# Kernel optimization log

Measured on AMD Instinct MI355X. Metric: run time of the kernel, lower is better.

Reference implementation:

```python
import jax, jax.numpy as jnp
import numpy as np

N = 50000      # nodes
E = 800000     # edges (avg degree 16)
F_IN = 256     # input feature dim
H, D = 4, 32   # heads, per-head dim
HD = H * D
K = 25000      # SAGPool keeps ceil(0.5*N) nodes
C = 2          # classes
SLOPE = 0.4
NEG = -1e9

def _gat(x, src, dst, valid, n, W, b, al, ar):
    # DGL GATConv: fc -> per-head attn logits -> edge softmax over dst -> weighted sum
    h = (x @ W).reshape(-1, H, D)                      # [n,H,D]
    el = jnp.einsum('nhd,hd->nh', h, al)
    er = jnp.einsum('nhd,hd->nh', h, ar)
    e = jax.nn.leaky_relu(el[src] + er[dst], SLOPE)    # [E,H]
    e = jnp.where(valid[:, None], e, NEG)
    m = jnp.maximum(jax.ops.segment_max(e, dst, num_segments=n), NEG)
    ex = jnp.exp(e - m[dst]) * valid[:, None].astype(x.dtype)
    s = jax.ops.segment_sum(ex, dst, num_segments=n)
    alpha = ex / jnp.maximum(s[dst], 1e-16)            # [E,H] edge softmax
    out = jax.ops.segment_sum(alpha[:, :, None] * h[src], dst, num_segments=n)
    return out + b.reshape(1, H, D), alpha

def _sagpool(x, src, dst, valid, n, k, Wc, bc):
    # score = GraphConv(in,1) with symmetric norm; keep top-k nodes, scale by tanh(score)
    vf = valid.astype(x.dtype)
    deg_o = jnp.maximum(jax.ops.segment_sum(vf, src, num_segments=n), 1.0)
    deg_i = jnp.maximum(jax.ops.segment_sum(vf, dst, num_segments=n), 1.0)
    h = (x @ Wc) * (deg_o ** -0.5)[:, None]
    agg = jax.ops.segment_sum(h[src] * vf[:, None], dst, num_segments=n)
    score = (agg * (deg_i ** -0.5)[:, None] + bc)[:, 0]   # [n]
    vals, perm = jax.lax.top_k(score, k)
    xk = x[perm] * jnp.tanh(vals)[:, None]                # [k,F]
    new_id = jnp.full((n,), -1, jnp.int32).at[perm].set(jnp.arange(k, dtype=jnp.int32))
    ns, nd = new_id[src], new_id[dst]
    nv = valid & (ns >= 0) & (nd >= 0)                    # edges fully inside subgraph
    return xk, jnp.where(nv, ns, 0), jnp.where(nv, nd, 0), nv

def setup_inputs():
    key = jax.random.key(0)
    k = jax.random.split(key, 18)
    rn = lambda i, shape, scale: jax.random.normal(k[i], shape, jnp.float32) * scale
    return {
        "feature": rn(0, (N, F_IN), 1.0),
        "strength": jax.random.uniform(k[1], (E,), dtype=jnp.float32),
        "W0": rn(2, (F_IN, HD), F_IN ** -0.5), "b0": jnp.zeros((HD,), jnp.float32),
        "al0": rn(3, (H, D), 0.1), "ar0": rn(4, (H, D), 0.1),
        "Wc0": rn(5, (HD, 1), HD ** -0.5), "bc0": jnp.zeros((1,), jnp.float32),
        "W1": rn(6, (HD, HD), HD ** -0.5), "b1": jnp.zeros((HD,), jnp.float32),
        "al1": rn(7, (H, D), 0.1), "ar1": rn(8, (H, D), 0.1),
        "gate_W": rn(9, (D, 1), D ** -0.5), "gate_b": jnp.zeros((1,), jnp.float32),
        "cls_W": rn(10, (D, C), D ** -0.5), "cls_b": jnp.zeros((C,), jnp.float32),
        "src": jax.random.randint(k[11], (E,), 0, N, dtype=jnp.int32),
        "dst": jax.random.randint(k[12], (E,), 0, N, dtype=jnp.int32),
    }

def reference(feature, strength, W0, b0, al0, ar0, Wc0, bc0, W1, b1, al1, ar1,
              gate_W, gate_b, cls_W, cls_b, src, dst):
    valid0 = jnp.ones((E,), bool)
    h0, _ = _gat(feature, src, dst, valid0, N, W0, b0, al0, ar0)
    x = h0.reshape(N, HD)                                  # flatten(1)
    x1, s1, d1, v1 = _sagpool(x, src, dst, valid0, N, K, Wc0, bc0)
    h1, atten = _gat(x1, s1, d1, v1, K, W1, b1, al1, ar1)  # get_attention=True
    strength1 = strength * v1.astype(strength.dtype)       # edata carried into subgraph (masked)
    res = h1.mean(axis=1)                                  # [K,D] mean over heads
    gate = jax.nn.softmax(res @ gate_W + gate_b, axis=0)   # [K,1] GlobalAttentionPooling
    readout = jnp.sum(gate * res, axis=0, keepdims=True)   # [1,D]
    lbl_pred = readout @ cls_W + cls_b                     # [1,C]
    return (readout, lbl_pred, atten, strength1)
```

## Files before the change

### kernel.cpp

```cpp
#include <hip/hip_runtime.h>
#include <stdint.h>

#define NN 50000
#define EE 800000
#define FIN 256
#define HD 128
#define DD 32
#define KK 25000
#define SLOPEF 0.4f
#define NEGF (-1e9f)
#define ATT_OFF 34
#define STR_OFF (34 + EE * 4)
#define CW 128

__device__ __forceinline__ unsigned fkey(float x) {
    unsigned u = __float_as_uint(x);
    return (u & 0x80000000u) ? ~u : (u | 0x80000000u);
}
__device__ __forceinline__ float unfkey(unsigned k) {
    unsigned u = (k & 0x80000000u) ? (k ^ 0x80000000u) : ~k;
    return __uint_as_float(u);
}
__device__ __forceinline__ float lrelu(float v) { return v > 0.f ? v : SLOPEF * v; }

struct P {
    const float *feature, *strength, *W0, *b0, *al0, *ar0, *Wc0, *bc0;
    const float *W1, *b1, *al1, *ar1, *gW, *gb, *cW, *cb;
    const int *src, *dst;
    double *Zacc, *racc;
    int *deg_i, *deg_o, *deg1, *cnt;
    unsigned *gmaxk, *rs;
    unsigned *binsHi, *binsLo;
    unsigned *keys;
    int *csr_src, *rank, *off0, *off1, *sel, *slot, *list, *bsum, *boff;
    float *z0, *el0, *er0, *q4, *m0f, *s0f, *b0wc, *hc, *score, *xk, *z1;
    float *el1, *er1, *m1f, *s1f, *res, *g, *tscale;
    float *out;
};

#define BM 128
#define BN 64
#define BK 16
__device__ void gemm_body(
    const float* __restrict__ A, const float* __restrict__ B, float* __restrict__ C,
    int M, int Kd,
    const float* __restrict__ al, const float* __restrict__ ar,
    float* __restrict__ el, float* __restrict__ er,
    const float* __restrict__ Wc, float* __restrict__ q4,
    int bx, int by) {
    __shared__ float As[BK][BM + 4];
    __shared__ float Bs[BK][BN];
    int bm = by * BM, bn = bx * BN;
    int tid = threadIdx.x;
    int tr = tid >> 4, tc = tid & 15;
    int lrow = tid >> 1;
    int arow = (bm + lrow < M) ? (bm + lrow) : -1;
    float acc[8][4] = {};
    for (int k0 = 0; k0 < Kd; k0 += BK) {
        {
            int col = (tid & 1) << 3;
            float4 v0 = {0.f,0.f,0.f,0.f}, v1 = {0.f,0.f,0.f,0.f};
            if (arow >= 0) {
                const float* ap = A + (size_t)arow * Kd + k0 + col;
                v0 = *(const float4*)ap; v1 = *(const float4*)(ap + 4);
            }
            As[col + 0][lrow] = v0.x; As[col + 1][lrow] = v0.y;
            As[col + 2][lrow] = v0.z; As[col + 3][lrow] = v0.w;
            As[col + 4][lrow] = v1.x; As[col + 5][lrow] = v1.y;
            As[col + 6][lrow] = v1.z; As[col + 7][lrow] = v1.w;
        }
        {
            int kr = tid >> 4, col = (tid & 15) << 2;
            float4 v = *(const float4*)(B + (size_t)(k0 + kr) * HD + bn + col);
            *(float4*)&Bs[kr][col] = v;
        }
        __syncthreads();
#pragma unroll
        for (int kk = 0; kk < BK; kk++) {
            float a[8], b[4];
#pragma unroll
            for (int i = 0; i < 8; i++) a[i] = As[kk][tr * 8 + i];
#pragma unroll
            for (int j = 0; j < 4; j++) b[j] = Bs[kk][tc * 4 + j];
#pragma unroll
            for (int i = 0; i < 8; i++)
#pragma unroll
                for (int j = 0; j < 4; j++) acc[i][j] = fmaf(a[i], b[j], acc[i][j]);
        }
        __syncthreads();
    }
#pragma unroll
    for (int i = 0; i < 8; i++) {
        int gr = bm + tr * 8 + i;
        if (gr < M) {
            float4 v = {acc[i][0], acc[i][1], acc[i][2], acc[i][3]};
            *(float4*)(C + (size_t)gr * HD + bn + tc * 4) = v;
        }
    }
    int head = bx * 2 + (tc >> 3);
    int dbase = (tc & 7) * 4;
    const float* alh = al + head * 32 + dbase;
    const float* arh = ar + head * 32 + dbase;
    float a0 = alh[0], a1 = alh[1], a2 = alh[2], a3 = alh[3];
    float r0 = arh[0], r1 = arh[1], r2 = arh[2], r3 = arh[3];
    float w0 = 0.f, w1 = 0.f, w2 = 0.f, w3 = 0.f;
    if (Wc) {
        const float* wch = Wc + head * 32 + dbase;
        w0 = wch[0]; w1 = wch[1]; w2 = wch[2]; w3 = wch[3];
    }
#pragma unroll
    for (int i = 0; i < 8; i++) {
        int gr = bm + tr * 8 + i;
        float pe = acc[i][0]*a0 + acc[i][1]*a1 + acc[i][2]*a2 + acc[i][3]*a3;
        float pr = acc[i][0]*r0 + acc[i][1]*r1 + acc[i][2]*r2 + acc[i][3]*r3;
        float pq = acc[i][0]*w0 + acc[i][1]*w1 + acc[i][2]*w2 + acc[i][3]*w3;
#pragma unroll
        for (int o = 1; o < 8; o <<= 1) {
            pe += __shfl_xor(pe, o); pr += __shfl_xor(pr, o); pq += __shfl_xor(pq, o);
        }
        if ((tc & 7) == 0 && gr < M) {
            el[gr * 4 + head] = pe; er[gr * 4 + head] = pr;
            if (Wc) q4[gr * 4 + head] = pq;
        }
    }
}

#define G0B 782
__global__ __launch_bounds__(256) void k_g0deg(P p) {
    int blk = blockIdx.x;
    if (blk < G0B) {
        gemm_body(p.feature, p.W0, p.z0, NN, FIN, p.al0, p.ar0, p.el0, p.er0,
                  p.Wc0, p.q4, blk & 1, blk >> 1);
    } else if (blk < G0B + 3125) {
        int e = (blk - G0B) * 256 + threadIdx.x;
        if (e < EE) {
            p.rank[e] = atomicAdd(&p.deg_i[p.dst[e]], 1);
            atomicAdd(&p.deg_o[p.src[e]], 1);
        }
    } else {
        int l = threadIdx.x;
        if (l < 64) {
            float t = p.b0[l] * p.Wc0[l] + p.b0[l + 64] * p.Wc0[l + 64];
#pragma unroll
            for (int o = 1; o < 64; o <<= 1) t += __shfl_xor(t, o);
            if (l == 0) p.b0wc[0] = t;
        }
    }
}

#define G1B 392
__global__ __launch_bounds__(256) void k_g1deg(P p) {
    int blk = blockIdx.x;
    if (blk < G1B) {
        gemm_body(p.xk, p.W1, p.z1, KK, HD, p.al1, p.ar1, p.el1, p.er1,
                  nullptr, nullptr, blk & 1, blk >> 1);
    } else {
        int e = (blk - G1B) * 256 + threadIdx.x;
        if (e < EE) {
            int ds = p.slot[p.src[e]], dd = p.slot[p.dst[e]];
            int r = -1;
            if (ds >= 0 && dd >= 0) r = atomicAdd(&p.deg1[dd], 1);
            p.rank[e] = r;
        }
    }
}

__global__ __launch_bounds__(256) void k_bsum(const int* __restrict__ deg,
                                              int* __restrict__ bsum, int n) {
    int i = blockIdx.x * 256 + threadIdx.x;
    int v = (i < n) ? deg[i] : 0;
    int lane = threadIdx.x & 63, w = threadIdx.x >> 6;
    __shared__ int ws[4];
#pragma unroll
    for (int o = 1; o < 64; o <<= 1) v += __shfl_xor(v, o);
    if (lane == 0) ws[w] = v;
    __syncthreads();
    if (threadIdx.x == 0) bsum[blockIdx.x] = ws[0] + ws[1] + ws[2] + ws[3];
}
__global__ __launch_bounds__(256) void k_bscan(const int* __restrict__ bsum, int nb,
                                               int* __restrict__ boff,
                                               int* __restrict__ off, int n) {
    __shared__ int ws[4];
    __shared__ int wo[5];
    int t = threadIdx.x;
    int v = (t < nb) ? bsum[t] : 0;
    int lane = t & 63, w = t >> 6;
    int incl = v;
    for (int o = 1; o < 64; o <<= 1) { int u = __shfl_up(incl, o); if (lane >= o) incl += u; }
    if (lane == 63) ws[w] = incl;
    __syncthreads();
    if (t == 0) { int a = 0; for (int i = 0; i < 4; i++) { wo[i] = a; a += ws[i]; } wo[4] = a; }
    __syncthreads();
    if (t < nb) boff[t] = wo[w] + incl - v;
    if (t == 0) off[n] = wo[4];
}
__global__ __launch_bounds__(256) void k_fscan(const int* __restrict__ deg,
                                               const int* __restrict__ boff,
                                               int* __restrict__ off, int n) {
    __shared__ int ws[4];
    __shared__ int wo[4];
    int i = blockIdx.x * 256 + threadIdx.x;
    int v = (i < n) ? deg[i] : 0;
    int lane = threadIdx.x & 63, w = threadIdx.x >> 6;
    int incl = v;
    for (int o = 1; o < 64; o <<= 1) { int u = __shfl_up(incl, o); if (lane >= o) incl += u; }
    if (lane == 63) ws[w] = incl;
    __syncthreads();
    if (threadIdx.x == 0) { int a = 0; for (int k = 0; k < 4; k++) { wo[k] = a; a += ws[k]; } }
    __syncthreads();
    if (i < n) off[i] = boff[blockIdx.x] + wo[w] + incl - v;
}

__global__ void k_scatter0(P p) {
    int e = blockIdx.x * blockDim.x + threadIdx.x;
    if (e >= EE) return;
    p.csr_src[p.off0[p.dst[e]] + p.rank[e]] = p.src[e];
}
__global__ void k_scatter1(P p) {
    int e = blockIdx.x * blockDim.x + threadIdx.x;
    if (e >= EE) return;
    int r = p.rank[e];
    if (r >= 0) {
        int dd = p.slot[p.dst[e]];
        p.csr_src[p.off1[dd] + r] = p.slot[p.src[e]];
    }
}

__global__ __launch_bounds__(256) void k_fgatlite(
    const int* __restrict__ off, const int* __restrict__ csrs,
    const float* __restrict__ el, const float* __restrict__ er,
    const float* __restrict__ q4, const int* __restrict__ dego,
    const float* __restrict__ b0wc,
    float* __restrict__ hc, float* __restrict__ m0f, float* __restrict__ s0f) {
    int wv = threadIdx.x >> 6, lane = threadIdx.x & 63;
    int v = blockIdx.x * 4 + wv;
    int b = off[v], e = off[v + 1], deg = e - b;
    int h = lane >> 4, sub = lane & 15;
    float erh = er[(size_t)v * 4 + h];
    float m = NEGF;
    for (int li = sub; li < deg; li += 16) {
        int s = csrs[b + li];
        m = fmaxf(m, lrelu(el[(size_t)s * 4 + h] + erh));
    }
#pragma unroll
    for (int o = 1; o < 16; o <<= 1) m = fmaxf(m, __shfl_xor(m, o));
    float ssum = 0.f, hq = 0.f;
    for (int li = sub; li < deg; li += 16) {
        int s = csrs[b + li];
        float ex = expf(lrelu(el[(size_t)s * 4 + h] + erh) - m);
        ssum += ex;
        hq = fmaf(ex, q4[(size_t)s * 4 + h], hq);
    }
#pragma unroll
    for (int o = 1; o < 16; o <<= 1) { ssum += __shfl_xor(ssum, o); hq += __shfl_xor(hq, o); }
    if (sub == 0) { m0f[v * 4 + h] = m; s0f[v * 4 + h] = ssum; }
    float t = hq / fmaxf(ssum, 1e-16f);
    t += __shfl_xor(t, 16);
    t += __shfl_xor(t, 32);
    if (lane == 0)
        hc[v] = (t + b0wc[0]) / sqrtf(fmaxf((float)dego[v], 1.f));
}

__global__ __launch_bounds__(256) void k_fgatx(
    const int* __restrict__ list, const float* __restrict__ tscale,
    const int* __restrict__ off, const int* __restrict__ csrs,
    const float* __restrict__ el, const float* __restrict__ er,
    const float* __restrict__ m0f, const float* __restrict__ s0f,
    const float* __restrict__ z, const float* __restrict__ b0,
    float* __restrict__ xk) {
    __shared__ int ssrc[4][CW];
    __shared__ float sexp[4][CW][4];
    int wv = threadIdx.x >> 6, lane = threadIdx.x & 63;
    int i = blockIdx.x * 4 + wv;
    int v = list[i];
    int b = off[v], e = off[v + 1], deg = e - b;
    int h = lane >> 4, sub = lane & 15;
    float erh = er[(size_t)v * 4 + h];
    float mh = m0f[v * 4 + h];
    for (int li = sub; li < deg; li += 16) {
        int s = csrs[b + li];
        if (h == 0 && li < CW) ssrc[wv][li] = s;
        if (li < CW) sexp[wv][li][h] = expf(lrelu(el[(size_t)s * 4 + h] + erh) - mh);
    }
    __syncthreads();
    int h0 = lane >> 5, h1 = h0 + 2;
    float s0 = s0f[v * 4 + h0], s1 = s0f[v * 4 + h1];
    float m0 = m0f[v * 4 + h0], m1 = m0f[v * 4 + h1];
    float er0v = er[(size_t)v * 4 + h0], er1v = er[(size_t)v * 4 + h1];
    int c0 = lane, c1 = lane + 64;
    float acc0 = 0.f, acc1 = 0.f;
    for (int li = 0; li < deg; li++) {
        int s; float w0, w1;
        if (li < CW) {
            s = ssrc[wv][li];
            w0 = sexp[wv][li][h0]; w1 = sexp[wv][li][h1];
        } else {
            s = csrs[b + li];
            w0 = expf(lrelu(el[(size_t)s * 4 + h0] + er0v) - m0);
            w1 = expf(lrelu(el[(size_t)s * 4 + h1] + er1v) - m1);
        }
        int su = __builtin_amdgcn_readfirstlane(s);
        const float* zr = z + (size_t)su * HD;
        acc0 = fmaf(w0, zr[c0], acc0);
        acc1 = fmaf(w1, zr[c1], acc1);
    }
    float ts = tscale[i];
    float* xr = xk + (size_t)i * HD;
    xr[c0] = (acc0 / fmaxf(s0, 1e-16f) + b0[c0]) * ts;
    xr[c1] = (acc1 / fmaxf(s1, 1e-16f) + b0[c1]) * ts;
}

__global__ void k_score(P p) {
    int v = blockIdx.x * blockDim.x + threadIdx.x;
    if (v >= NN) return;
    int b = p.off0[v], en = p.off0[v + 1];
    float acc = 0.f;
    for (int i = b; i < en; i++) acc += p.hc[p.csr_src[i]];
    float dg = fmaxf((float)(en - b), 1.f);
    float sc = acc / sqrtf(dg) + p.bc0[0];
    p.score[v] = sc;
    p.keys[v] = fkey(sc);
}

__global__ void k_hist2(P p, int level) {
    int v = blockIdx.x * blockDim.x + threadIdx.x;
    if (v >= NN) return;
    unsigned key = p.keys[v];
    if (level == 0) atomicAdd(&p.binsHi[key >> 16], 1u);
    else if ((key >> 16) == p.rs[2]) atomicAdd(&p.binsLo[key & 0xFFFFu], 1u);
}
__global__ __launch_bounds__(1024) void k_rsel2(P p, int level) {
    const unsigned* bins = level ? p.binsLo : p.binsHi;
    int K = level ? (int)p.rs[3] : KK;
    __shared__ unsigned wsm[16];
    __shared__ unsigned wpre[17];
    int t = threadIdx.x;
    unsigned base = (unsigned)t * 64;
    const uint4* b4 = (const uint4*)(bins + base);
    unsigned S = 0;
#pragma unroll
    for (int i = 0; i < 16; i++) {
        uint4 u = b4[i];
        S += u.x + u.y + u.z + u.w;
    }
    int lane = t & 63, w = t >> 6;
    unsigned val = S;
    for (int o = 1; o < 64; o <<= 1) { unsigned u = __shfl_up(val, o); if (lane >= o) val += u; }
    if (lane == 63) wsm[w] = val;
    __syncthreads();
    if (t == 0) { unsigned a = 0; for (int i = 0; i < 16; i++) { wpre[i] = a; a += wsm[i]; } wpre[16] = a; }
    __syncthreads();
    unsigned incl = wpre[w] + val;
    unsigned running = wpre[16] - incl;
    for (int i = 63; i >= 0; i--) {
        unsigned c = bins[base + i];
        unsigned above = running;
        running += c;
        if ((int)above < K && (int)running >= K) {
            if (level == 0) { p.rs[2] = base + (unsigned)i; p.rs[3] = (unsigned)(K - (int)above); }
            else { p.rs[0] = (p.rs[2] << 16) | (base + (unsigned)i); p.rs[1] = (unsigned)(K - (int)above); }
        }
    }
}
__global__ void k_sel(P p) {
    int v = blockIdx.x * blockDim.x + threadIdx.x;
    if (v >= NN) return;
    p.sel[v] = (p.keys[v] > p.rs[0]) ? 1 : 0;
}
__global__ __launch_bounds__(1024) void k_ties(P p) {
    __shared__ int base;
    __shared__ int wsums[16];
    unsigned pivot = p.rs[0];
    int need = (int)p.rs[1];
    if (threadIdx.x == 0) base = 0;
    __syncthreads();
    for (int st = 0; st < NN; st += 1024) {
        int v = st + (int)threadIdx.x;
        int flag = (v < NN && p.keys[v] == pivot) ? 1 : 0;
        unsigned long long m = __ballot(flag);
        int lane = threadIdx.x & 63, w = threadIdx.x >> 6;
        int pre = __popcll(m & ((1ull << lane) - 1ull));
        if (lane == 0) wsums[w] = __popcll(m);
        __syncthreads();
        int woff = 0;
        for (int i = 0; i < w; i++) woff += wsums[i];
        int rank = base + woff + pre;
        if (flag && rank < need) p.sel[v] = 1;
        __syncthreads();
        if (threadIdx.x == 0) {
            int s = 0;
            for (int i = 0; i < 16; i++) s += wsums[i];
            base += s;
        }
        __syncthreads();
    }
}
__global__ void k_list(P p) {
    int v = blockIdx.x * blockDim.x + threadIdx.x;
    if (v >= NN) return;
    if (p.sel[v]) {
        int i = atomicAdd(p.cnt, 1);
        p.list[i] = v;
        p.slot[v] = i;
        p.tscale[i] = tanhf(p.score[v]);
    } else {
        p.slot[v] = -1;
    }
}

__global__ __launch_bounds__(256) void k_fgat2(
    const int* __restrict__ off, const int* __restrict__ csrs,
    const float* __restrict__ el, const float* __restrict__ er,
    const float* __restrict__ z, const float* __restrict__ bias,
    float* __restrict__ mf, float* __restrict__ sf,
    const float* __restrict__ gW, const float* __restrict__ gb,
    float* __restrict__ res, float* __restrict__ g) {
    __shared__ int ssrc[4][CW];
    __shared__ float sexp[4][CW][4];
    int wv = threadIdx.x >> 6, lane = threadIdx.x & 63;
    int v = blockIdx.x * 4 + wv;
    int b = off[v], e = off[v + 1], deg = e - b;
    int h = lane >> 4, sub = lane & 15;
    float4 er4 = *(const float4*)(er + (size_t)v * 4);
    float erh = ((const float*)&er4)[h];
    float m = NEGF;
    for (int li = sub; li < deg; li += 16) {
        int s = csrs[b + li];
        if (h == 0 && li < CW) ssrc[wv][li] = s;
        m = fmaxf(m, lrelu(el[(size_t)s * 4 + h] + erh));
    }
#pragma unroll
    for (int o = 1; o < 16; o <<= 1) m = fmaxf(m, __shfl_xor(m, o));
    float ssum = 0.f;
    for (int li = sub; li < deg; li += 16) {
        int s = csrs[b + li];
        float x = expf(lrelu(el[(size_t)s * 4 + h] + erh) - m);
        if (li < CW) sexp[wv][li][h] = x;
        ssum += x;
    }
#pragma unroll
    for (int o = 1; o < 16; o <<= 1) ssum += __shfl_xor(ssum, o);
    if (sub == 0) { mf[v * 4 + h] = m; sf[v * 4 + h] = ssum; }
    __syncthreads();
    int h0 = lane >> 5, h1 = h0 + 2;
    float m0 = __shfl(m, h0 << 4), m1 = __shfl(m, h1 << 4);
    float s0 = __shfl(ssum, h0 << 4), s1 = __shfl(ssum, h1 << 4);
    int c0 = lane, c1 = lane + 64;
    float acc0 = 0.f, acc1 = 0.f;
    for (int li = 0; li < deg; li++) {
        int s; float w0, w1;
        if (li < CW) {
            s = ssrc[wv][li];
            w0 = sexp[wv][li][h0]; w1 = sexp[wv][li][h1];
        } else {
            s = csrs[b + li];
            w0 = expf(lrelu(el[(size_t)s * 4 + h0] + ((const float*)&er4)[h0]) - m0);
            w1 = expf(lrelu(el[(size_t)s * 4 + h1] + ((const float*)&er4)[h1]) - m1);
        }
        int su = __builtin_amdgcn_readfirstlane(s);
        const float* zr = z + (size_t)su * HD;
        acc0 = fmaf(w0, zr[c0], acc0);
        acc1 = fmaf(w1, zr[c1], acc1);
    }
    float xc0 = acc0 / fmaxf(s0, 1e-16f) + bias[c0];
    float xc1 = acc1 / fmaxf(s1, 1e-16f) + bias[c1];
    float t = xc0 + xc1;
    t += __shfl_xor(t, 32);
    float pg = 0.f;
    if (lane < 32) {
        float r = 0.25f * t;
        res[(size_t)v * 32 + lane] = r;
        pg = r * gW[lane];
    }
#pragma unroll
    for (int o = 1; o < 32; o <<= 1) pg += __shfl_xor(pg, o);
    if (lane == 0) g[v] = pg + gb[0];
}

__global__ void k_ealpha1(P p) {
    int e = blockIdx.x * blockDim.x + threadIdx.x;
    if (e >= EE) return;
    int ds = p.slot[p.src[e]], dd = p.slot[p.dst[e]];
    float a[4] = {0.f, 0.f, 0.f, 0.f};
    float st = 0.f;
    if (ds >= 0 && dd >= 0) {
        float4 es = *(const float4*)(p.el1 + ds * 4);
        float4 ed = *(const float4*)(p.er1 + dd * 4);
        float l[4] = {lrelu(es.x + ed.x), lrelu(es.y + ed.y), lrelu(es.z + ed.z), lrelu(es.w + ed.w)};
#pragma unroll
        for (int h = 0; h < 4; h++) {
            float m = p.m1f[dd * 4 + h];
            float ex = expf(l[h] - m);
            a[h] = ex / fmaxf(p.s1f[dd * 4 + h], 1e-16f);
        }
        st = p.strength[e];
    }
    float* o = p.out + ATT_OFF + (size_t)e * 4;
    *(float2*)(o) = make_float2(a[0], a[1]);
    *(float2*)(o + 2) = make_float2(a[2], a[3]);
    p.out[STR_OFF + e] = st;
}

__global__ void k_gmax(P p) {
    __shared__ float red[256];
    int t = threadIdx.x;
    float m = -3.4e38f;
    for (int i = blockIdx.x * 256 + t; i < KK; i += gridDim.x * 256) m = fmaxf(m, p.g[i]);
    red[t] = m;
    __syncthreads();
    for (int o = 128; o > 0; o >>= 1) { if (t < o) red[t] = fmaxf(red[t], red[t + o]); __syncthreads(); }
    if (t == 0) atomicMax(p.gmaxk, fkey(red[0]));
}
#define WSUM_BLOCKS 104
__global__ __launch_bounds__(256) void k_wsum(P p) {
    __shared__ double vred[256];
    __shared__ double zred[8];
    int t = threadIdx.x, il = t >> 5, d = t & 31;
    float gm = unfkey(*p.gmaxk);
    double accv = 0.0, accw = 0.0;
    for (int i = blockIdx.x * 8 + il; i < KK; i += WSUM_BLOCKS * 8) {
        float w = expf(p.g[i] - gm);
        accv += (double)(w * p.res[(size_t)i * 32 + d]);
        if (d == 0) accw += (double)w;
    }
    vred[t] = accv;
    if (d == 0) zred[il] = accw;
    __syncthreads();
    if (il == 0) {
        double s = 0;
#pragma unroll
        for (int k2 = 0; k2 < 8; k2++) s += vred[k2 * 32 + d];
        atomicAdd(&p.racc[d], s);
    }
    if (t == 32) {
        double z2 = 0;
#pragma unroll
        for (int k2 = 0; k2 < 8; k2++) z2 += zred[k2];
        atomicAdd(p.Zacc, z2);
    }
}
__global__ void k_final(P p) {
    __shared__ float rb[32];
    int t = threadIdx.x;
    double Z = *p.Zacc;
    if (t < 32) {
        float r = (float)(p.racc[t] / Z);
        p.out[t] = r;
        rb[t] = r;
    }
    __syncthreads();
    if (t < 2) {
        float s = 0.f;
        for (int d = 0; d < 32; d++) s += rb[d] * p.cW[d * 2 + t];
        p.out[32 + t] = s + p.cb[t];
    }
}

extern "C" void kernel_launch(void* const* d_in, const int* in_sizes, int n_in,
                              void* d_out, int out_size, void* d_ws, size_t ws_size,
                              hipStream_t stream) {
    (void)in_sizes; (void)n_in; (void)out_size; (void)ws_size;
    P p;
    p.feature  = (const float*)d_in[0];
    p.strength = (const float*)d_in[1];
    p.W0  = (const float*)d_in[2];  p.b0  = (const float*)d_in[3];
    p.al0 = (const float*)d_in[4];  p.ar0 = (const float*)d_in[5];
    p.Wc0 = (const float*)d_in[6];  p.bc0 = (const float*)d_in[7];
    p.W1  = (const float*)d_in[8];  p.b1  = (const float*)d_in[9];
    p.al1 = (const float*)d_in[10]; p.ar1 = (const float*)d_in[11];
    p.gW  = (const float*)d_in[12]; p.gb  = (const float*)d_in[13];
    p.cW  = (const float*)d_in[14]; p.cb  = (const float*)d_in[15];
    p.src = (const int*)d_in[16];   p.dst = (const int*)d_in[17];
    p.out = (float*)d_out;

    char* ws = (char*)d_ws;
    size_t off = 0;
    auto alloc = [&](size_t bytes) -> void* {
        void* r = ws + off;
        off = (off + bytes + 255) & ~(size_t)255;
        return r;
    };
    p.Zacc  = (double*)alloc(8);
    p.racc  = (double*)alloc(32 * 8);
    p.deg_i = (int*)alloc((size_t)NN * 4);
    p.deg_o = (int*)alloc((size_t)NN * 4);
    p.deg1  = (int*)alloc((size_t)KK * 4);
    p.cnt   = (int*)alloc(4);
    p.gmaxk = (unsigned*)alloc(4);
    p.rs    = (unsigned*)alloc(16);
    p.binsHi = (unsigned*)alloc(65536 * 4);
    p.binsLo = (unsigned*)alloc(65536 * 4);
    size_t zbytes = off;
    p.z0 = (float*)alloc((size_t)NN * HD * 4);
    p.xk = (float*)alloc((size_t)KK * HD * 4);
    p.z1 = (float*)alloc((size_t)KK * HD * 4);
    p.csr_src = (int*)alloc((size_t)EE * 4);
    p.rank    = (int*)alloc((size_t)EE * 4);
    p.el0 = (float*)alloc((size_t)NN * 4 * 4);
    p.er0 = (float*)alloc((size_t)NN * 4 * 4);
    p.q4  = (float*)alloc((size_t)NN * 4 * 4);
    p.m0f = (float*)alloc((size_t)NN * 4 * 4);
    p.s0f = (float*)alloc((size_t)NN * 4 * 4);
    p.b0wc = (float*)alloc(4);
    p.off0 = (int*)alloc((size_t)(NN + 1) * 4);
    p.off1 = (int*)alloc((size_t)(KK + 1) * 4);
    p.bsum = (int*)alloc(256 * 4);
    p.boff = (int*)alloc(256 * 4);
    p.hc    = (float*)alloc((size_t)NN * 4);
    p.score = (float*)alloc((size_t)NN * 4);
    p.keys  = (unsigned*)alloc((size_t)NN * 4);
    p.sel   = (int*)alloc((size_t)NN * 4);
    p.slot  = (int*)alloc((size_t)NN * 4);
    p.list  = (int*)alloc((size_t)KK * 4);
    p.tscale = (float*)alloc((size_t)KK * 4);
    p.el1 = (float*)alloc((size_t)KK * 4 * 4);
    p.er1 = (float*)alloc((size_t)KK * 4 * 4);
    p.m1f = (float*)alloc((size_t)KK * 4 * 4);
    p.s1f = (float*)alloc((size_t)KK * 4 * 4);
    p.res = (float*)alloc((size_t)KK * DD * 4);
    p.g   = (float*)alloc((size_t)KK * 4);

    const int GB_E = (EE + 255) / 256;
    const int GB_N = (NN + 255) / 256;
    const int GB_K = (KK + 255) / 256;

    hipMemsetAsync(d_ws, 0, zbytes, stream);

    k_g0deg<<<G0B + GB_E + 1, 256, 0, stream>>>(p);
    k_bsum<<<GB_N, 256, 0, stream>>>(p.deg_i, p.bsum, NN);
    k_bscan<<<1, 256, 0, stream>>>(p.bsum, GB_N, p.boff, p.off0, NN);
    k_fscan<<<GB_N, 256, 0, stream>>>(p.deg_i, p.boff, p.off0, NN);
    k_scatter0<<<GB_E, 256, 0, stream>>>(p);
    k_fgatlite<<<NN / 4, 256, 0, stream>>>(p.off0, p.csr_src, p.el0, p.er0, p.q4,
                                           p.deg_o, p.b0wc, p.hc, p.m0f, p.s0f);

    k_score<<<GB_N, 256, 0, stream>>>(p);
    k_hist2<<<GB_N, 256, 0, stream>>>(p, 0);
    k_rsel2<<<1, 1024, 0, stream>>>(p, 0);
    k_hist2<<<GB_N, 256, 0, stream>>>(p, 1);
    k_rsel2<<<1, 1024, 0, stream>>>(p, 1);
    k_sel<<<GB_N, 256, 0, stream>>>(p);
    k_ties<<<1, 1024, 0, stream>>>(p);
    k_list<<<GB_N, 256, 0, stream>>>(p);
    k_fgatx<<<KK / 4, 256, 0, stream>>>(p.list, p.tscale, p.off0, p.csr_src,
                                        p.el0, p.er0, p.m0f, p.s0f, p.z0, p.b0, p.xk);

    k_g1deg<<<G1B + GB_E, 256, 0, stream>>>(p);
    k_bsum<<<GB_K, 256, 0, stream>>>(p.deg1, p.bsum, KK);
    k_bscan<<<1, 256, 0, stream>>>(p.bsum, GB_K, p.boff, p.off1, KK);
    k_fscan<<<GB_K, 256, 0, stream>>>(p.deg1, p.boff, p.off1, KK);
    k_scatter1<<<GB_E, 256, 0, stream>>>(p);
    k_fgat2<<<KK / 4, 256, 0, stream>>>(p.off1, p.csr_src, p.el1, p.er1, p.z1, p.b1,
                                        p.m1f, p.s1f, p.gW, p.gb, p.res, p.g);
    k_ealpha1<<<GB_E, 256, 0, stream>>>(p);

    k_gmax<<<98, 256, 0, stream>>>(p);
    k_wsum<<<WSUM_BLOCKS, 256, 0, stream>>>(p);
    k_final<<<1, 64, 0, stream>>>(p);
}
```

Measured before the change: 588.1 us.

## Build CSR with node-range partitioned LDS histograms instead of global atomics

```diff
diff --git a/kernel.cpp b/kernel.cpp
--- a/kernel.cpp
+++ b/kernel.cpp
@@ -13,6 +13,12 @@
 #define STR_OFF (34 + EE * 4)
 #define CW 128
 
+#define NCB 64
+#define ECB 4
+#define CH0 782
+#define CH1 391
+#define ECHUNK4 (EE / ECB / 4)
+
 __device__ __forceinline__ unsigned fkey(float x) {
     unsigned u = __float_as_uint(x);
     return (u & 0x80000000u) ? ~u : (u | 0x80000000u);
@@ -28,11 +34,13 @@
     const float *W1, *b1, *al1, *ar1, *gW, *gb, *cW, *cb;
     const int *src, *dst;
     double *Zacc, *racc;
-    int *deg_i, *deg_o, *deg1, *cnt;
+    int *cnt;
     unsigned *gmaxk, *rs;
     unsigned *binsHi, *binsLo;
     unsigned *keys;
-    int *csr_src, *rank, *off0, *off1, *sel, *slot, *list, *bsum, *boff;
+    int *degc_i, *degc_o, *degc1;
+    int *ens, *end_;
+    int *csr_src, *off0, *off1, *sel, *slot, *list, *bsum, *boff;
     float *z0, *el0, *er0, *q4, *m0f, *s0f, *b0wc, *hc, *score, *xk, *z1;
     float *el1, *er1, *m1f, *s1f, *res, *g, *tscale;
     float *out;
@@ -131,11 +139,35 @@
     if (blk < G0B) {
         gemm_body(p.feature, p.W0, p.z0, NN, FIN, p.al0, p.ar0, p.el0, p.er0,
                   p.Wc0, p.q4, blk & 1, blk >> 1);
-    } else if (blk < G0B + 3125) {
-        int e = (blk - G0B) * 256 + threadIdx.x;
-        if (e < EE) {
-            p.rank[e] = atomicAdd(&p.deg_i[p.dst[e]], 1);
-            atomicAdd(&p.deg_o[p.src[e]], 1);
+    } else if (blk < G0B + NCB * ECB) {
+        int cb = blk - G0B;
+        int r = cb & (NCB - 1), c = cb >> 6;
+        int base = r * CH0;
+        __shared__ unsigned cnti[CH0], cnto[CH0];
+        for (int v = threadIdx.x; v < CH0; v += 256) { cnti[v] = 0u; cnto[v] = 0u; }
+        __syncthreads();
+        const int4* s4 = (const int4*)p.src;
+        const int4* d4 = (const int4*)p.dst;
+        int j0 = c * ECHUNK4, j1 = j0 + ECHUNK4;
+        for (int j = j0 + (int)threadIdx.x; j < j1; j += 256) {
+            int4 dv = d4[j], sv = s4[j];
+            unsigned t;
+            t = (unsigned)(dv.x - base); if (t < (unsigned)CH0) atomicAdd(&cnti[t], 1u);
+            t = (unsigned)(dv.y - base); if (t < (unsigned)CH0) atomicAdd(&cnti[t], 1u);
+            t = (unsigned)(dv.z - base); if (t < (unsigned)CH0) atomicAdd(&cnti[t], 1u);
+            t = (unsigned)(dv.w - base); if (t < (unsigned)CH0) atomicAdd(&cnti[t], 1u);
+            t = (unsigned)(sv.x - base); if (t < (unsigned)CH0) atomicAdd(&cnto[t], 1u);
+            t = (unsigned)(sv.y - base); if (t < (unsigned)CH0) atomicAdd(&cnto[t], 1u);
+            t = (unsigned)(sv.z - base); if (t < (unsigned)CH0) atomicAdd(&cnto[t], 1u);
+            t = (unsigned)(sv.w - base); if (t < (unsigned)CH0) atomicAdd(&cnto[t], 1u);
+        }
+        __syncthreads();
+        for (int v = threadIdx.x; v < CH0; v += 256) {
+            int node = base + v;
+            if (node < NN) {
+                p.degc_i[(size_t)c * NN + node] = (int)cnti[v];
+                p.degc_o[(size_t)c * NN + node] = (int)cnto[v];
+            }
         }
     } else {
         int l = threadIdx.x;
@@ -146,6 +178,15 @@
             if (l == 0) p.b0wc[0] = t;
         }
     }
+}
+
+__global__ void k_emap(P p) {
+    int e = blockIdx.x * blockDim.x + threadIdx.x;
+    if (e >= EE) return;
+    int ns = p.slot[p.src[e]], nd = p.slot[p.dst[e]];
+    if (ns < 0) nd = -1;
+    p.ens[e] = ns;
+    p.end_[e] = nd;
 }
 
 #define G1B 392
@@ -155,20 +196,38 @@
         gemm_body(p.xk, p.W1, p.z1, KK, HD, p.al1, p.ar1, p.el1, p.er1,
                   nullptr, nullptr, blk & 1, blk >> 1);
     } else {
-        int e = (blk - G1B) * 256 + threadIdx.x;
-        if (e < EE) {
-            int ds = p.slot[p.src[e]], dd = p.slot[p.dst[e]];
-            int r = -1;
-            if (ds >= 0 && dd >= 0) r = atomicAdd(&p.deg1[dd], 1);
-            p.rank[e] = r;
+        int cb = blk - G1B;
+        int r = cb & (NCB - 1), c = cb >> 6;
+        int base = r * CH1;
+        __shared__ unsigned cnt1[CH1];
+        for (int v = threadIdx.x; v < CH1; v += 256) cnt1[v] = 0u;
+        __syncthreads();
+        const int4* d4 = (const int4*)p.end_;
+        int j0 = c * ECHUNK4, j1 = j0 + ECHUNK4;
+        for (int j = j0 + (int)threadIdx.x; j < j1; j += 256) {
+            int4 dv = d4[j];
+            unsigned t;
+            t = (unsigned)(dv.x - base); if (t < (unsigned)CH1) atomicAdd(&cnt1[t], 1u);
+            t = (unsigned)(dv.y - base); if (t < (unsigned)CH1) atomicAdd(&cnt1[t], 1u);
+            t = (unsigned)(dv.z - base); if (t < (unsigned)CH1) atomicAdd(&cnt1[t], 1u);
+            t = (unsigned)(dv.w - base); if (t < (unsigned)CH1) atomicAdd(&cnt1[t], 1u);
+        }
+        __syncthreads();
+        for (int v = threadIdx.x; v < CH1; v += 256) {
+            int node = base + v;
+            if (node < KK) p.degc1[(size_t)c * KK + node] = (int)cnt1[v];
         }
     }
 }
 
 __global__ __launch_bounds__(256) void k_bsum(const int* __restrict__ deg,
-                                              int* __restrict__ bsum, int n) {
+                                              int* __restrict__ bsum, int n, int nn) {
     int i = blockIdx.x * 256 + threadIdx.x;
-    int v = (i < n) ? deg[i] : 0;
+    int v = 0;
+    if (i < n) {
+#pragma unroll
+        for (int c = 0; c < ECB; c++) v += deg[(size_t)c * nn + i];
+    }
     int lane = threadIdx.x & 63, w = threadIdx.x >> 6;
     __shared__ int ws[4];
 #pragma unroll
@@ -196,11 +255,15 @@
 }
 __global__ __launch_bounds__(256) void k_fscan(const int* __restrict__ deg,
                                                const int* __restrict__ boff,
-                                               int* __restrict__ off, int n) {
+                                               int* __restrict__ off, int n, int nn) {
     __shared__ int ws[4];
     __shared__ int wo[4];
     int i = blockIdx.x * 256 + threadIdx.x;
-    int v = (i < n) ? deg[i] : 0;
+    int v = 0;
+    if (i < n) {
+#pragma unroll
+        for (int c = 0; c < ECB; c++) v += deg[(size_t)c * nn + i];
+    }
     int lane = threadIdx.x & 63, w = threadIdx.x >> 6;
     int incl = v;
     for (int o = 1; o < 64; o <<= 1) { int u = __shfl_up(incl, o); if (lane >= o) incl += u; }
@@ -211,25 +274,63 @@
     if (i < n) off[i] = boff[blockIdx.x] + wo[w] + incl - v;
 }
 
-__global__ void k_scatter0(P p) {
-    int e = blockIdx.x * blockDim.x + threadIdx.x;
-    if (e >= EE) return;
-    p.csr_src[p.off0[p.dst[e]] + p.rank[e]] = p.src[e];
-}
-__global__ void k_scatter1(P p) {
-    int e = blockIdx.x * blockDim.x + threadIdx.x;
-    if (e >= EE) return;
-    int r = p.rank[e];
-    if (r >= 0) {
-        int dd = p.slot[p.dst[e]];
-        p.csr_src[p.off1[dd] + r] = p.slot[p.src[e]];
+__global__ __launch_bounds__(256) void k_scatter0(P p) {
+    int cb = blockIdx.x;
+    int r = cb & (NCB - 1), c = cb >> 6;
+    int base = r * CH0;
+    __shared__ unsigned cur[CH0];
+    for (int v = threadIdx.x; v < CH0; v += 256) {
+        int node = base + v;
+        if (node < NN) {
+            unsigned o = (unsigned)p.off0[node];
+            for (int cc = 0; cc < c; cc++) o += (unsigned)p.degc_i[(size_t)cc * NN + node];
+            cur[v] = o;
+        }
+    }
+    __syncthreads();
+    const int4* s4 = (const int4*)p.src;
+    const int4* d4 = (const int4*)p.dst;
+    int j0 = c * ECHUNK4, j1 = j0 + ECHUNK4;
+    for (int j = j0 + (int)threadIdx.x; j < j1; j += 256) {
+        int4 dv = d4[j], sv = s4[j];
+        unsigned t, pos;
+        t = (unsigned)(dv.x - base); if (t < (unsigned)CH0) { pos = atomicAdd(&cur[t], 1u); p.csr_src[pos] = sv.x; }
+        t = (unsigned)(dv.y - base); if (t < (unsigned)CH0) { pos = atomicAdd(&cur[t], 1u); p.csr_src[pos] = sv.y; }
+        t = (unsigned)(dv.z - base); if (t < (unsigned)CH0) { pos = atomicAdd(&cur[t], 1u); p.csr_src[pos] = sv.z; }
+        t = (unsigned)(dv.w - base); if (t < (unsigned)CH0) { pos = atomicAdd(&cur[t], 1u); p.csr_src[pos] = sv.w; }
+    }
+}
+__global__ __launch_bounds__(256) void k_scatter1(P p) {
+    int cb = blockIdx.x;
+    int r = cb & (NCB - 1), c = cb >> 6;
+    int base = r * CH1;
+    __shared__ unsigned cur[CH1];
+    for (int v = threadIdx.x; v < CH1; v += 256) {
+        int node = base + v;
+        if (node < KK) {
+            unsigned o = (unsigned)p.off1[node];
+            for (int cc = 0; cc < c; cc++) o += (unsigned)p.degc1[(size_t)cc * KK + node];
+            cur[v] = o;
+        }
+    }
+    __syncthreads();
+    const int4* s4 = (const int4*)p.ens;
+    const int4* d4 = (const int4*)p.end_;
+    int j0 = c * ECHUNK4, j1 = j0 + ECHUNK4;
+    for (int j = j0 + (int)threadIdx.x; j < j1; j += 256) {
+        int4 dv = d4[j], sv = s4[j];
+        unsigned t, pos;
+        t = (unsigned)(dv.x - base); if (t < (unsigned)CH1) { pos = atomicAdd(&cur[t], 1u); p.csr_src[pos] = sv.x; }
+        t = (unsigned)(dv.y - base); if (t < (unsigned)CH1) { pos = atomicAdd(&cur[t], 1u); p.csr_src[pos] = sv.y; }
+        t = (unsigned)(dv.z - base); if (t < (unsigned)CH1) { pos = atomicAdd(&cur[t], 1u); p.csr_src[pos] = sv.z; }
+        t = (unsigned)(dv.w - base); if (t < (unsigned)CH1) { pos = atomicAdd(&cur[t], 1u); p.csr_src[pos] = sv.w; }
     }
 }
 
 __global__ __launch_bounds__(256) void k_fgatlite(
     const int* __restrict__ off, const int* __restrict__ csrs,
     const float* __restrict__ el, const float* __restrict__ er,
-    const float* __restrict__ q4, const int* __restrict__ dego,
+    const float* __restrict__ q4, const int* __restrict__ degco,
     const float* __restrict__ b0wc,
     float* __restrict__ hc, float* __restrict__ m0f, float* __restrict__ s0f) {
     int wv = threadIdx.x >> 6, lane = threadIdx.x & 63;
@@ -257,8 +358,10 @@
     float t = hq / fmaxf(ssum, 1e-16f);
     t += __shfl_xor(t, 16);
     t += __shfl_xor(t, 32);
-    if (lane == 0)
-        hc[v] = (t + b0wc[0]) / sqrtf(fmaxf((float)dego[v], 1.f));
+    if (lane == 0) {
+        int dv = degco[v] + degco[NN + v] + degco[2 * NN + v] + degco[3 * NN + v];
+        hc[v] = (t + b0wc[0]) / sqrtf(fmaxf((float)dv, 1.f));
+    }
 }
 
 __global__ __launch_bounds__(256) void k_fgatx(
@@ -480,10 +583,10 @@
 __global__ void k_ealpha1(P p) {
     int e = blockIdx.x * blockDim.x + threadIdx.x;
     if (e >= EE) return;
-    int ds = p.slot[p.src[e]], dd = p.slot[p.dst[e]];
+    int ds = p.ens[e], dd = p.end_[e];
     float a[4] = {0.f, 0.f, 0.f, 0.f};
     float st = 0.f;
-    if (ds >= 0 && dd >= 0) {
+    if (dd >= 0) {
         float4 es = *(const float4*)(p.el1 + ds * 4);
         float4 ed = *(const float4*)(p.er1 + dd * 4);
         float l[4] = {lrelu(es.x + ed.x), lrelu(es.y + ed.y), lrelu(es.z + ed.z), lrelu(es.w + ed.w)};
@@ -582,20 +685,21 @@
     };
     p.Zacc  = (double*)alloc(8);
     p.racc  = (double*)alloc(32 * 8);
-    p.deg_i = (int*)alloc((size_t)NN * 4);
-    p.deg_o = (int*)alloc((size_t)NN * 4);
-    p.deg1  = (int*)alloc((size_t)KK * 4);
     p.cnt   = (int*)alloc(4);
     p.gmaxk = (unsigned*)alloc(4);
     p.rs    = (unsigned*)alloc(16);
     p.binsHi = (unsigned*)alloc(65536 * 4);
     p.binsLo = (unsigned*)alloc(65536 * 4);
     size_t zbytes = off;
+    p.degc_i = (int*)alloc((size_t)ECB * NN * 4);
+    p.degc_o = (int*)alloc((size_t)ECB * NN * 4);
+    p.degc1  = (int*)alloc((size_t)ECB * KK * 4);
+    p.ens    = (int*)alloc((size_t)EE * 4);
+    p.end_   = (int*)alloc((size_t)EE * 4);
     p.z0 = (float*)alloc((size_t)NN * HD * 4);
     p.xk = (float*)alloc((size_t)KK * HD * 4);
     p.z1 = (float*)alloc((size_t)KK * HD * 4);
     p.csr_src = (int*)alloc((size_t)EE * 4);
-    p.rank    = (int*)alloc((size_t)EE * 4);
     p.el0 = (float*)alloc((size_t)NN * 4 * 4);
     p.er0 = (float*)alloc((size_t)NN * 4 * 4);
     p.q4  = (float*)alloc((size_t)NN * 4 * 4);
@@ -626,13 +730,13 @@
 
     hipMemsetAsync(d_ws, 0, zbytes, stream);
 
-    k_g0deg<<<G0B + GB_E + 1, 256, 0, stream>>>(p);
-    k_bsum<<<GB_N, 256, 0, stream>>>(p.deg_i, p.bsum, NN);
+    k_g0deg<<<G0B + NCB * ECB + 1, 256, 0, stream>>>(p);
+    k_bsum<<<GB_N, 256, 0, stream>>>(p.degc_i, p.bsum, NN, NN);
     k_bscan<<<1, 256, 0, stream>>>(p.bsum, GB_N, p.boff, p.off0, NN);
-    k_fscan<<<GB_N, 256, 0, stream>>>(p.deg_i, p.boff, p.off0, NN);
-    k_scatter0<<<GB_E, 256, 0, stream>>>(p);
+    k_fscan<<<GB_N, 256, 0, stream>>>(p.degc_i, p.boff, p.off0, NN, NN);
+    k_scatter0<<<NCB * ECB, 256, 0, stream>>>(p);
     k_fgatlite<<<NN / 4, 256, 0, stream>>>(p.off0, p.csr_src, p.el0, p.er0, p.q4,
-                                           p.deg_o, p.b0wc, p.hc, p.m0f, p.s0f);
+                                           p.degc_o, p.b0wc, p.hc, p.m0f, p.s0f);
 
     k_score<<<GB_N, 256, 0, stream>>>(p);
     k_hist2<<<GB_N, 256, 0, stream>>>(p, 0);
@@ -642,14 +746,15 @@
     k_sel<<<GB_N, 256, 0, stream>>>(p);
     k_ties<<<1, 1024, 0, stream>>>(p);
     k_list<<<GB_N, 256, 0, stream>>>(p);
+    k_emap<<<GB_E, 256, 0, stream>>>(p);
     k_fgatx<<<KK / 4, 256, 0, stream>>>(p.list, p.tscale, p.off0, p.csr_src,
                                         p.el0, p.er0, p.m0f, p.s0f, p.z0, p.b0, p.xk);
 
-    k_g1deg<<<G1B + GB_E, 256, 0, stream>>>(p);
-    k_bsum<<<GB_K, 256, 0, stream>>>(p.deg1, p.bsum, KK);
+    k_g1deg<<<G1B + NCB * ECB, 256, 0, stream>>>(p);
+    k_bsum<<<GB_K, 256, 0, stream>>>(p.degc1, p.bsum, KK, KK);
     k_bscan<<<1, 256, 0, stream>>>(p.bsum, GB_K, p.boff, p.off1, KK);
-    k_fscan<<<GB_K, 256, 0, stream>>>(p.deg1, p.boff, p.off1, KK);
-    k_scatter1<<<GB_E, 256, 0, stream>>>(p);
+    k_fscan<<<GB_K, 256, 0, stream>>>(p.degc1, p.boff, p.off1, KK, KK);
+    k_scatter1<<<NCB * ECB, 256, 0, stream>>>(p);
     k_fgat2<<<KK / 4, 256, 0, stream>>>(p.off1, p.csr_src, p.el1, p.er1, p.z1, p.b1,
                                         p.m1f, p.s1f, p.gW, p.gb, p.res, p.g);
     k_ealpha1<<<GB_E, 256, 0, stream>>>(p);
```

Result: slower. 864.5 us (+47.0%).

## Build CSR with per-chunk LDS byte histograms and fuse scatter into GEMM launches

Applied to the files above, without the earlier changes.

```diff
diff --git a/kernel.cpp b/kernel.cpp
--- a/kernel.cpp
+++ b/kernel.cpp
@@ -13,6 +13,9 @@
 #define STR_OFF (34 + EE * 4)
 #define CW 128
 
+#define BCH 32
+#define EPC (EE / BCH)
+
 __device__ __forceinline__ unsigned fkey(float x) {
     unsigned u = __float_as_uint(x);
     return (u & 0x80000000u) ? ~u : (u | 0x80000000u);
@@ -28,10 +31,14 @@
     const float *W1, *b1, *al1, *ar1, *gW, *gb, *cW, *cb;
     const int *src, *dst;
     double *Zacc, *racc;
-    int *deg_i, *deg_o, *deg1, *cnt;
+    int *cnt;
     unsigned *gmaxk, *rs;
     unsigned *binsHi, *binsLo;
     unsigned *keys;
+    unsigned char *degc_i, *degc_o, *degc1;
+    unsigned *cb0, *cb1;
+    int *dsum;
+    int *ens, *end_;
     int *csr_src, *rank, *off0, *off1, *sel, *slot, *list, *bsum, *boff;
     float *z0, *el0, *er0, *q4, *m0f, *s0f, *b0wc, *hc, *score, *xk, *z1;
     float *el1, *er1, *m1f, *s1f, *res, *g, *tscale;
@@ -125,50 +132,68 @@
     }
 }
 
-#define G0B 782
-__global__ __launch_bounds__(256) void k_g0deg(P p) {
+__global__ __launch_bounds__(256) void k_count0(P p) {
+    __shared__ unsigned hist[NN / 4];
     int blk = blockIdx.x;
-    if (blk < G0B) {
-        gemm_body(p.feature, p.W0, p.z0, NN, FIN, p.al0, p.ar0, p.el0, p.er0,
-                  p.Wc0, p.q4, blk & 1, blk >> 1);
-    } else if (blk < G0B + 3125) {
-        int e = (blk - G0B) * 256 + threadIdx.x;
-        if (e < EE) {
-            p.rank[e] = atomicAdd(&p.deg_i[p.dst[e]], 1);
-            atomicAdd(&p.deg_o[p.src[e]], 1);
+    int isD = blk < BCH;
+    int c = isD ? blk : blk - BCH;
+    for (int w = threadIdx.x; w < NN / 4; w += 256) hist[w] = 0u;
+    __syncthreads();
+    int j0 = c * EPC, j1 = j0 + EPC;
+    if (isD) {
+        for (int e = j0 + (int)threadIdx.x; e < j1; e += 256) {
+            int d = p.dst[e];
+            unsigned sh = (unsigned)(d & 3) * 8u;
+            unsigned old = atomicAdd(&hist[d >> 2], 1u << sh);
+            p.rank[e] = (int)((old >> sh) & 0xffu);
         }
     } else {
-        int l = threadIdx.x;
-        if (l < 64) {
-            float t = p.b0[l] * p.Wc0[l] + p.b0[l + 64] * p.Wc0[l + 64];
-#pragma unroll
-            for (int o = 1; o < 64; o <<= 1) t += __shfl_xor(t, o);
-            if (l == 0) p.b0wc[0] = t;
-        }
-    }
-}
-
-#define G1B 392
-__global__ __launch_bounds__(256) void k_g1deg(P p) {
-    int blk = blockIdx.x;
-    if (blk < G1B) {
-        gemm_body(p.xk, p.W1, p.z1, KK, HD, p.al1, p.ar1, p.el1, p.er1,
-                  nullptr, nullptr, blk & 1, blk >> 1);
-    } else {
-        int e = (blk - G1B) * 256 + threadIdx.x;
-        if (e < EE) {
-            int ds = p.slot[p.src[e]], dd = p.slot[p.dst[e]];
-            int r = -1;
-            if (ds >= 0 && dd >= 0) r = atomicAdd(&p.deg1[dd], 1);
-            p.rank[e] = r;
-        }
-    }
-}
-
-__global__ __launch_bounds__(256) void k_bsum(const int* __restrict__ deg,
-                                              int* __restrict__ bsum, int n) {
+        for (int e = j0 + (int)threadIdx.x; e < j1; e += 256) {
+            int s = p.src[e];
+            atomicAdd(&hist[s >> 2], 1u << ((unsigned)(s & 3) * 8u));
+        }
+    }
+    __syncthreads();
+    unsigned* o32 = (unsigned*)((isD ? p.degc_i : p.degc_o) + (size_t)c * NN);
+    for (int w = threadIdx.x; w < NN / 4; w += 256) o32[w] = hist[w];
+}
+
+__global__ __launch_bounds__(256) void k_count1(P p) {
+    __shared__ unsigned hist[KK / 4];
+    int c = blockIdx.x;
+    for (int w = threadIdx.x; w < KK / 4; w += 256) hist[w] = 0u;
+    __syncthreads();
+    int j0 = c * EPC, j1 = j0 + EPC;
+    for (int e = j0 + (int)threadIdx.x; e < j1; e += 256) {
+        int d = p.end_[e];
+        if (d >= 0) {
+            unsigned sh = (unsigned)(d & 3) * 8u;
+            unsigned old = atomicAdd(&hist[d >> 2], 1u << sh);
+            p.rank[e] = (int)((old >> sh) & 0xffu);
+        }
+    }
+    __syncthreads();
+    unsigned* o32 = (unsigned*)(p.degc1 + (size_t)c * KK);
+    for (int w = threadIdx.x; w < KK / 4; w += 256) o32[w] = hist[w];
+}
+
+__global__ void k_emap(P p) {
+    int e = blockIdx.x * blockDim.x + threadIdx.x;
+    if (e >= EE) return;
+    int ns = p.slot[p.src[e]], nd = p.slot[p.dst[e]];
+    if (ns < 0) nd = -1;
+    p.ens[e] = ns;
+    p.end_[e] = nd;
+}
+
+__global__ __launch_bounds__(256) void k_bsum(const unsigned char* __restrict__ deg,
+                                              int* __restrict__ bsum, int n, int nn) {
     int i = blockIdx.x * 256 + threadIdx.x;
-    int v = (i < n) ? deg[i] : 0;
+    int v = 0;
+    if (i < n) {
+#pragma unroll
+        for (int c = 0; c < BCH; c++) v += deg[(size_t)c * nn + i];
+    }
     int lane = threadIdx.x & 63, w = threadIdx.x >> 6;
     __shared__ int ws[4];
 #pragma unroll
@@ -194,13 +219,15 @@
     if (t < nb) boff[t] = wo[w] + incl - v;
     if (t == 0) off[n] = wo[4];
 }
-__global__ __launch_bounds__(256) void k_fscan(const int* __restrict__ deg,
-                                               const int* __restrict__ boff,
-                                               int* __restrict__ off, int n) {
+__global__ __launch_bounds__(256) void k_fscan0(P p) {
     __shared__ int ws[4];
     __shared__ int wo[4];
     int i = blockIdx.x * 256 + threadIdx.x;
-    int v = (i < n) ? deg[i] : 0;
+    int v = 0;
+    if (i < NN) {
+#pragma unroll
+        for (int c = 0; c < BCH; c++) v += p.degc_i[(size_t)c * NN + i];
+    }
     int lane = threadIdx.x & 63, w = threadIdx.x >> 6;
     int incl = v;
     for (int o = 1; o < 64; o <<= 1) { int u = __shfl_up(incl, o); if (lane >= o) incl += u; }
@@ -208,28 +235,97 @@
     __syncthreads();
     if (threadIdx.x == 0) { int a = 0; for (int k = 0; k < 4; k++) { wo[k] = a; a += ws[k]; } }
     __syncthreads();
-    if (i < n) off[i] = boff[blockIdx.x] + wo[w] + incl - v;
-}
-
-__global__ void k_scatter0(P p) {
-    int e = blockIdx.x * blockDim.x + threadIdx.x;
-    if (e >= EE) return;
-    p.csr_src[p.off0[p.dst[e]] + p.rank[e]] = p.src[e];
-}
-__global__ void k_scatter1(P p) {
-    int e = blockIdx.x * blockDim.x + threadIdx.x;
-    if (e >= EE) return;
-    int r = p.rank[e];
-    if (r >= 0) {
-        int dd = p.slot[p.dst[e]];
-        p.csr_src[p.off1[dd] + r] = p.slot[p.src[e]];
+    if (i < NN) {
+        int base = p.boff[blockIdx.x] + wo[w] + incl - v;
+        p.off0[i] = base;
+        unsigned run = (unsigned)base;
+        int s = 0;
+#pragma unroll
+        for (int c = 0; c < BCH; c++) {
+            p.cb0[(size_t)c * NN + i] = run;
+            run += p.degc_i[(size_t)c * NN + i];
+            s += p.degc_o[(size_t)c * NN + i];
+        }
+        p.dsum[i] = s;
+    }
+}
+__global__ __launch_bounds__(256) void k_fscan1(P p) {
+    __shared__ int ws[4];
+    __shared__ int wo[4];
+    int i = blockIdx.x * 256 + threadIdx.x;
+    int v = 0;
+    if (i < KK) {
+#pragma unroll
+        for (int c = 0; c < BCH; c++) v += p.degc1[(size_t)c * KK + i];
+    }
+    int lane = threadIdx.x & 63, w = threadIdx.x >> 6;
+    int incl = v;
+    for (int o = 1; o < 64; o <<= 1) { int u = __shfl_up(incl, o); if (lane >= o) incl += u; }
+    if (lane == 63) ws[w] = incl;
+    __syncthreads();
+    if (threadIdx.x == 0) { int a = 0; for (int k = 0; k < 4; k++) { wo[k] = a; a += ws[k]; } }
+    __syncthreads();
+    if (i < KK) {
+        int base = p.boff[blockIdx.x] + wo[w] + incl - v;
+        p.off1[i] = base;
+        unsigned run = (unsigned)base;
+#pragma unroll
+        for (int c = 0; c < BCH; c++) {
+            p.cb1[(size_t)c * KK + i] = run;
+            run += p.degc1[(size_t)c * KK + i];
+        }
+    }
+}
+
+#define G0B 782
+#define GB_E 3125
+__global__ __launch_bounds__(256) void k_g0sc(P p) {
+    int blk = blockIdx.x;
+    if (blk < G0B) {
+        gemm_body(p.feature, p.W0, p.z0, NN, FIN, p.al0, p.ar0, p.el0, p.er0,
+                  p.Wc0, p.q4, blk & 1, blk >> 1);
+    } else if (blk < G0B + GB_E) {
+        int e = (blk - G0B) * 256 + threadIdx.x;
+        if (e < EE) {
+            int c = e / EPC;
+            int d = p.dst[e];
+            unsigned pos = p.cb0[(size_t)c * NN + d] + (unsigned)p.rank[e];
+            p.csr_src[pos] = p.src[e];
+        }
+    } else {
+        int l = threadIdx.x;
+        if (l < 64) {
+            float t = p.b0[l] * p.Wc0[l] + p.b0[l + 64] * p.Wc0[l + 64];
+#pragma unroll
+            for (int o = 1; o < 64; o <<= 1) t += __shfl_xor(t, o);
+            if (l == 0) p.b0wc[0] = t;
+        }
+    }
+}
+
+#define G1B 392
+__global__ __launch_bounds__(256) void k_g1sc(P p) {
+    int blk = blockIdx.x;
+    if (blk < G1B) {
+        gemm_body(p.xk, p.W1, p.z1, KK, HD, p.al1, p.ar1, p.el1, p.er1,
+                  nullptr, nullptr, blk & 1, blk >> 1);
+    } else {
+        int e = (blk - G1B) * 256 + threadIdx.x;
+        if (e < EE) {
+            int d = p.end_[e];
+            if (d >= 0) {
+                int c = e / EPC;
+                unsigned pos = p.cb1[(size_t)c * KK + d] + (unsigned)p.rank[e];
+                p.csr_src[pos] = p.ens[e];
+            }
+        }
     }
 }
 
 __global__ __launch_bounds__(256) void k_fgatlite(
     const int* __restrict__ off, const int* __restrict__ csrs,
     const float* __restrict__ el, const float* __restrict__ er,
-    const float* __restrict__ q4, const int* __restrict__ dego,
+    const float* __restrict__ q4, const int* __restrict__ dsum,
     const float* __restrict__ b0wc,
     float* __restrict__ hc, float* __restrict__ m0f, float* __restrict__ s0f) {
     int wv = threadIdx.x >> 6, lane = threadIdx.x & 63;
@@ -258,7 +354,7 @@
     t += __shfl_xor(t, 16);
     t += __shfl_xor(t, 32);
     if (lane == 0)
-        hc[v] = (t + b0wc[0]) / sqrtf(fmaxf((float)dego[v], 1.f));
+        hc[v] = (t + b0wc[0]) / sqrtf(fmaxf((float)dsum[v], 1.f));
 }
 
 __global__ __launch_bounds__(256) void k_fgatx(
@@ -480,10 +576,10 @@
 __global__ void k_ealpha1(P p) {
     int e = blockIdx.x * blockDim.x + threadIdx.x;
     if (e >= EE) return;
-    int ds = p.slot[p.src[e]], dd = p.slot[p.dst[e]];
+    int ds = p.ens[e], dd = p.end_[e];
     float a[4] = {0.f, 0.f, 0.f, 0.f};
     float st = 0.f;
-    if (ds >= 0 && dd >= 0) {
+    if (dd >= 0) {
         float4 es = *(const float4*)(p.el1 + ds * 4);
         float4 ed = *(const float4*)(p.er1 + dd * 4);
         float l[4] = {lrelu(es.x + ed.x), lrelu(es.y + ed.y), lrelu(es.z + ed.z), lrelu(es.w + ed.w)};
@@ -582,15 +678,20 @@
     };
     p.Zacc  = (double*)alloc(8);
     p.racc  = (double*)alloc(32 * 8);
-    p.deg_i = (int*)alloc((size_t)NN * 4);
-    p.deg_o = (int*)alloc((size_t)NN * 4);
-    p.deg1  = (int*)alloc((size_t)KK * 4);
     p.cnt   = (int*)alloc(4);
     p.gmaxk = (unsigned*)alloc(4);
     p.rs    = (unsigned*)alloc(16);
     p.binsHi = (unsigned*)alloc(65536 * 4);
     p.binsLo = (unsigned*)alloc(65536 * 4);
     size_t zbytes = off;
+    p.degc_i = (unsigned char*)alloc((size_t)BCH * NN);
+    p.degc_o = (unsigned char*)alloc((size_t)BCH * NN);
+    p.degc1  = p.degc_i;
+    p.cb0 = (unsigned*)alloc((size_t)BCH * NN * 4);
+    p.cb1 = p.cb0;
+    p.dsum = (int*)alloc((size_t)NN * 4);
+    p.ens  = (int*)alloc((size_t)EE * 4);
+    p.end_ = (int*)alloc((size_t)EE * 4);
     p.z0 = (float*)alloc((size_t)NN * HD * 4);
     p.xk = (float*)alloc((size_t)KK * HD * 4);
     p.z1 = (float*)alloc((size_t)KK * HD * 4);
@@ -620,19 +721,18 @@
     p.res = (float*)alloc((size_t)KK * DD * 4);
     p.g   = (float*)alloc((size_t)KK * 4);
 
-    const int GB_E = (EE + 255) / 256;
     const int GB_N = (NN + 255) / 256;
     const int GB_K = (KK + 255) / 256;
 
     hipMemsetAsync(d_ws, 0, zbytes, stream);
 
-    k_g0deg<<<G0B + GB_E + 1, 256, 0, stream>>>(p);
-    k_bsum<<<GB_N, 256, 0, stream>>>(p.deg_i, p.bsum, NN);
+    k_count0<<<2 * BCH, 256, 0, stream>>>(p);
+    k_bsum<<<GB_N, 256, 0, stream>>>(p.degc_i, p.bsum, NN, NN);
     k_bscan<<<1, 256, 0, stream>>>(p.bsum, GB_N, p.boff, p.off0, NN);
-    k_fscan<<<GB_N, 256, 0, stream>>>(p.deg_i, p.boff, p.off0, NN);
-    k_scatter0<<<GB_E, 256, 0, stream>>>(p);
+    k_fscan0<<<GB_N, 256, 0, stream>>>(p);
+    k_g0sc<<<G0B + GB_E + 1, 256, 0, stream>>>(p);
     k_fgatlite<<<NN / 4, 256, 0, stream>>>(p.off0, p.csr_src, p.el0, p.er0, p.q4,
-                                           p.deg_o, p.b0wc, p.hc, p.m0f, p.s0f);
+                                           p.dsum, p.b0wc, p.hc, p.m0f, p.s0f);
 
     k_score<<<GB_N, 256, 0, stream>>>(p);
     k_hist2<<<GB_N, 256, 0, stream>>>(p, 0);
@@ -642,14 +742,15 @@
     k_sel<<<GB_N, 256, 0, stream>>>(p);
     k_ties<<<1, 1024, 0, stream>>>(p);
     k_list<<<GB_N, 256, 0, stream>>>(p);
+
+    k_emap<<<GB_E, 256, 0, stream>>>(p);
+    k_count1<<<BCH, 256, 0, stream>>>(p);
+    k_bsum<<<GB_K, 256, 0, stream>>>(p.degc1, p.bsum, KK, KK);
+    k_bscan<<<1, 256, 0, stream>>>(p.bsum, GB_K, p.boff, p.off1, KK);
+    k_fscan1<<<GB_K, 256, 0, stream>>>(p);
     k_fgatx<<<KK / 4, 256, 0, stream>>>(p.list, p.tscale, p.off0, p.csr_src,
                                         p.el0, p.er0, p.m0f, p.s0f, p.z0, p.b0, p.xk);
-
-    k_g1deg<<<G1B + GB_E, 256, 0, stream>>>(p);
-    k_bsum<<<GB_K, 256, 0, stream>>>(p.deg1, p.bsum, KK);
-    k_bscan<<<1, 256, 0, stream>>>(p.bsum, GB_K, p.boff, p.off1, KK);
-    k_fscan<<<GB_K, 256, 0, stream>>>(p.deg1, p.boff, p.off1, KK);
-    k_scatter1<<<GB_E, 256, 0, stream>>>(p);
+    k_g1sc<<<G1B + GB_E, 256, 0, stream>>>(p);
     k_fgat2<<<KK / 4, 256, 0, stream>>>(p.off1, p.csr_src, p.el1, p.er1, p.z1, p.b1,
                                         p.m1f, p.s1f, p.gW, p.gb, p.res, p.g);
     k_ealpha1<<<GB_E, 256, 0, stream>>>(p);
```

After: 630.0 us. 1.07x slower.
